# Performance work log

Hardware: AMD Instinct MI355X
Metric: run time of the kernel (lower is better)

## Reference

```python
import jax, jax.numpy as jnp
from jax import lax
import numpy as np

V, B, E, H, T = 32000, 32, 64, 256, 128
START = 0


def setup_inputs() -> dict:
    key = jax.random.key(0)
    ks = jax.random.split(key, 17)
    s = 0.1  # keep logits in a sane range
    inp = {
        "input_x": jax.random.randint(ks[0], (B, T), 0, V, dtype=jnp.int32),
        "emb": jax.random.normal(ks[1], (V, E), jnp.float32) * s,
        "Wi": jax.random.normal(ks[2], (E, H), jnp.float32) * s,
        "Ui": jax.random.normal(ks[3], (H, H), jnp.float32) * s,
        "bi": jax.random.normal(ks[4], (H,), jnp.float32) * s,
        "Wf": jax.random.normal(ks[5], (E, H), jnp.float32) * s,
        "Uf": jax.random.normal(ks[6], (H, H), jnp.float32) * s,
        "bf": jax.random.normal(ks[7], (H,), jnp.float32) * s,
        "Wog": jax.random.normal(ks[8], (E, H), jnp.float32) * s,
        "Uog": jax.random.normal(ks[9], (H, H), jnp.float32) * s,
        "bog": jax.random.normal(ks[10], (H,), jnp.float32) * s,
        "Wc": jax.random.normal(ks[11], (E, H), jnp.float32) * s,
        "Uc": jax.random.normal(ks[12], (H, H), jnp.float32) * s,
        "bc": jax.random.normal(ks[13], (H,), jnp.float32) * s,
        "Wo": jax.random.normal(ks[14], (H, V), jnp.float32) * s,
        "bo": jax.random.normal(ks[15], (V,), jnp.float32) * s,
        "start_token": START,
    }
    return inp


def reference(input_x, emb, Wi, Ui, bi, Wf, Uf, bf, Wog, Uog, bog,
              Wc, Uc, bc, Wo, bo, start_token):
    b, t = input_x.shape
    h_dim = Ui.shape[0]
    # teacher-forcing inputs: [start_emb, emb(x_0..x_{T-2})], time-major [T,B,E]
    x0 = emb[jnp.full((b,), start_token, dtype=jnp.int32)]  # [B,E]
    emb_x = jnp.transpose(emb[input_x], (1, 0, 2))          # [T,B,E]
    xs = jnp.concatenate([x0[None], emb_x[:-1]], axis=0)    # [T,B,E]

    def step(carry, x):
        h, c = carry
        i = jax.nn.sigmoid(x @ Wi + h @ Ui + bi)
        f = jax.nn.sigmoid(x @ Wf + h @ Uf + bf)
        o = jax.nn.sigmoid(x @ Wog + h @ Uog + bog)
        c_bar = jnp.tanh(x @ Wc + h @ Uc + bc)
        c = f * c + i * c_bar
        h = o * jnp.tanh(c)
        logits = h @ Wo + bo                                # [B,V]
        return (h, c), jax.nn.log_softmax(logits, axis=-1)

    h0 = jnp.zeros((b, h_dim), jnp.float32)
    _, logp = lax.scan(step, (h0, h0), xs)                  # [T,B,V]
    logp = jnp.transpose(logp, (1, 0, 2))                   # [B,T,V]
    # -sum over all tokens of log p(target); equals one_hot * log(softmax) sum
    tgt_logp = jnp.take_along_axis(logp, input_x[..., None].astype(jnp.int32), axis=-1)[..., 0]
    return -jnp.sum(tgt_logp)
```

## Files before the change

kernel.cpp:

```cpp
#include <hip/hip_runtime.h>
#include <hip/hip_bf16.h>
#include <math.h>

#define V 32000
#define B 32
#define E 64
#define H 256
#define T 128
#define NROW (B*T)
#define NC 128
#define NVB (V/NC)

typedef __attribute__((ext_vector_type(8))) short bf16x8;
typedef __attribute__((ext_vector_type(4))) float f32x4;
typedef __attribute__((ext_vector_type(8))) unsigned short u16x8;

#define OFF_XS   0
#define OFF_XW   (OFF_XS + NROW*E)
#define OFF_HB   (OFF_XW + NROW*4*H)
#define OFF_PS   (OFF_HB + NROW*H/2)
#define OFF_TL   (OFF_PS + NVB*NROW)
#define OFF_U8   (OFF_TL + NROW)
#define OFF_SC   (OFF_U8 + H*H)
#define OFF_TGT  (OFF_SC + 16)

static __device__ __forceinline__ unsigned short f2bf(float f) {
    union { float f; unsigned int u; } x; x.f = f;
    unsigned int r = x.u + 0x7fffu + ((x.u >> 16) & 1u);
    return (unsigned short)(r >> 16);
}
static __device__ __forceinline__ float bf2f(unsigned short u) {
    union { unsigned int u; float f; } x; x.u = ((unsigned int)u) << 16; return x.f;
}
static __device__ __forceinline__ float sigmoidf_(float x) { return 1.f / (1.f + __expf(-x)); }
static __device__ __forceinline__ float tanhf_(float x)    { return 2.f / (1.f + __expf(-2.f * x)) - 1.f; }

#if defined(__has_builtin)
#if __has_builtin(__builtin_amdgcn_sdot4)
#define HAVE_SDOT4 1
#endif
#endif
static __device__ __forceinline__ int dot4i8(unsigned int a, unsigned int b, int c) {
#ifdef HAVE_SDOT4
    return __builtin_amdgcn_sdot4((int)a, (int)b, c, false);
#else
    c += (int)(char)(a)       * (int)(char)(b);
    c += (int)(char)(a >> 8)  * (int)(char)(b >> 8);
    c += (int)(char)(a >> 16) * (int)(char)(b >> 16);
    c += (int)(char)(a >> 24) * (int)(char)(b >> 24);
    return c;
#endif
}

__global__ void lstm_embed(const int* __restrict__ x, const float* __restrict__ emb,
                           const int* __restrict__ start, float* __restrict__ xs,
                           float* __restrict__ out, int* __restrict__ tgtrow) {
    int idx = blockIdx.x * 256 + threadIdx.x;
    if (idx == 0) out[0] = 0.f;
    if (idx < NROW) tgtrow[idx] = x[(idx & 31) * T + (idx >> 5)];
    if (idx >= T * B * E) return;
    int t   = idx / (B * E);
    int rem = idx - t * (B * E);
    int b   = rem >> 6;
    int e   = rem & 63;
    int tok = (t == 0) ? start[0] : x[b * T + (t - 1)];
    xs[idx] = emb[tok * E + e];
}

__global__ __launch_bounds__(256) void lstm_xw(
        const float* __restrict__ xs, unsigned short* __restrict__ xwq,
        const float* __restrict__ Wi, const float* __restrict__ Wf,
        const float* __restrict__ Wog, const float* __restrict__ Wc,
        const float* __restrict__ bi, const float* __restrict__ bf,
        const float* __restrict__ bog, const float* __restrict__ bc) {
    __shared__ float xsl[32][65];
    const int t = blockIdx.x, tid = threadIdx.x;
    for (int i = tid; i < 32 * 64; i += 256) {
        int b = i >> 6, e = i & 63;
        xsl[b][e] = xs[(size_t)(t * 32 + b) * 64 + e];
    }
    __syncthreads();
    const int b = tid & 31, jg = tid >> 5;
    for (int jj = 0; jj < 32; ++jj) {
        const int j = jg * 32 + jj;
        float a0 = bi[j], a1 = bf[j], a2 = bog[j], a3 = bc[j];
        #pragma unroll 8
        for (int e = 0; e < E; ++e) {
            float xe = xsl[b][e];
            a0 += xe * Wi [e * H + j];
            a1 += xe * Wf [e * H + j];
            a2 += xe * Wog[e * H + j];
            a3 += xe * Wc [e * H + j];
        }
        ushort4 v;
        v.x = f2bf(a0); v.y = f2bf(a1); v.z = f2bf(a2); v.w = f2bf(a3);
        *(ushort4*)(xwq + ((size_t)(t * 32 + b) * 256 + j) * 4) = v;
    }
}

__global__ __launch_bounds__(256) void lstm_umax(
        const float* __restrict__ Ui, const float* __restrict__ Uf,
        const float* __restrict__ Uog, const float* __restrict__ Uc,
        float* __restrict__ sc) {
    const int g = blockIdx.x;
    const float* U = (g == 0) ? Ui : (g == 1) ? Uf : (g == 2) ? Uog : Uc;
    float m = 0.f;
    for (int i = threadIdx.x; i < H * H; i += 256) m = fmaxf(m, fabsf(U[i]));
    __shared__ float red[256];
    red[threadIdx.x] = m;
    __syncthreads();
    for (int off = 128; off > 0; off >>= 1) {
        if (threadIdx.x < off) red[threadIdx.x] = fmaxf(red[threadIdx.x], red[threadIdx.x + off]);
        __syncthreads();
    }
    if (threadIdx.x == 0) sc[g] = fmaxf(red[0], 1e-20f);
}

__global__ __launch_bounds__(256) void lstm_uq8(
        const float* __restrict__ Ui, const float* __restrict__ Uf,
        const float* __restrict__ Uog, const float* __restrict__ Uc,
        const float* __restrict__ sc, unsigned int* __restrict__ UQ8) {
    const int idx = blockIdx.x * 256 + threadIdx.x;
    const int k4 = idx >> 8, j = idx & 255;
    float inv[4] = { 127.f / sc[0], 127.f / sc[1], 127.f / sc[2], 127.f / sc[3] };
    const float* Ug[4] = { Ui, Uf, Uog, Uc };
    uint4 out;
    unsigned int* op = (unsigned int*)&out;
    #pragma unroll
    for (int g = 0; g < 4; ++g) {
        unsigned int w = 0;
        #pragma unroll
        for (int kk = 0; kk < 4; ++kk) {
            float v = Ug[g][(size_t)(k4 * 4 + kk) * H + j];
            int q = __float2int_rn(v * inv[g]);
            q = q > 127 ? 127 : (q < -127 ? -127 : q);
            w |= ((unsigned int)(q & 255)) << (kk * 8);
        }
        op[g] = w;
    }
    *(uint4*)(UQ8 + (size_t)idx * 4) = out;
}

__global__ __launch_bounds__(1024) void lstm_recur_i8(
        const unsigned short* __restrict__ xwq, const uint4* __restrict__ UQ8,
        const float* __restrict__ sc, unsigned short* __restrict__ hb) {
    __shared__ unsigned int hq8[2][64];
    __shared__ int4 red[4][256];
    const int b = blockIdx.x, tid = threadIdx.x;
    const int j = tid & 255, q = tid >> 8;
    const float f0 = sc[0] * (1.f / 16129.f), f1 = sc[1] * (1.f / 16129.f);
    const float f2 = sc[2] * (1.f / 16129.f), f3 = sc[3] * (1.f / 16129.f);
    float c_ = 0.f;

    for (int t = 0; t < T; ++t) {
        if (t > 0) {
            const uint4* up = UQ8 + (size_t)(q * 16) * 256 + j;
            const unsigned int* hrow = hq8[t & 1] + q * 16;
            int a0 = 0, a1 = 0, a2 = 0, a3 = 0;
            #pragma unroll
            for (int m = 0; m < 16; ++m) {
                uint4 u = up[(size_t)m * 256];
                unsigned int hv = hrow[m];
                a0 = dot4i8(u.x, hv, a0);
                a1 = dot4i8(u.y, hv, a1);
                a2 = dot4i8(u.z, hv, a2);
                a3 = dot4i8(u.w, hv, a3);
            }
            red[q][j] = make_int4(a0, a1, a2, a3);
        }
        __syncthreads();
        if (tid < 256) {
            ushort4 xw = *(const ushort4*)(xwq + ((size_t)(t * 32 + b) * 256 + j) * 4);
            float pi = bf2f(xw.x), pf = bf2f(xw.y), po = bf2f(xw.z), pc = bf2f(xw.w);
            if (t > 0) {
                int4 r0 = red[0][j], r1 = red[1][j], r2 = red[2][j], r3 = red[3][j];
                pi += (float)(r0.x + r1.x + r2.x + r3.x) * f0;
                pf += (float)(r0.y + r1.y + r2.y + r3.y) * f1;
                po += (float)(r0.z + r1.z + r2.z + r3.z) * f2;
                pc += (float)(r0.w + r1.w + r2.w + r3.w) * f3;
            }
            c_ = sigmoidf_(pf) * c_ + sigmoidf_(pi) * tanhf_(pc);
            float h = sigmoidf_(po) * tanhf_(c_);
            hb[(size_t)(t * B + b) * H + j] = f2bf(h);
            ((char*)hq8[(t + 1) & 1])[j] = (char)__float2int_rn(h * 127.f);
        }
        __syncthreads();
    }
}

__global__ __launch_bounds__(256) void lstm_wot(const float* __restrict__ Wo,
                                                unsigned short* __restrict__ WoT) {
    __shared__ unsigned short tle[64][65];
    const int n0 = blockIdx.x * 64, k0 = blockIdx.y * 64;
    const int tid = threadIdx.x;
    for (int i = tid; i < 64 * 64; i += 256) {
        int kk = i >> 6, nn = i & 63;
        tle[kk][nn] = f2bf(Wo[(size_t)(k0 + kk) * V + n0 + nn]);
    }
    __syncthreads();
    for (int c = tid; c < 512; c += 256) {
        int nn = c >> 3, kc = c & 7;
        u16x8 v;
        #pragma unroll
        for (int e = 0; e < 8; ++e) v[e] = tle[kc * 8 + e][nn];
        *(u16x8*)(WoT + (size_t)(n0 + nn) * H + k0 + kc * 8) = v;
    }
}

__global__ __launch_bounds__(512, 2) void lstm_logits_mfma(
        const unsigned short* __restrict__ hb, const unsigned short* __restrict__ WoT,
        const float* __restrict__ bo, const int* __restrict__ tgtrow,
        float* __restrict__ ps, float* __restrict__ tl) {
    __shared__ char a_s[65536];
    __shared__ char b_s[65536];
    __shared__ float s_red[4][128];
    __shared__ int   tgt_l[128];
    const int tid = threadIdx.x, lane = tid & 63, wid = tid >> 6;
    const int wr = wid >> 2, wc = wid & 3;
    const int lr = lane & 15, lg = lane >> 4;
    const int swz = lr & 7;
    const int vb = blockIdx.x * NC;

    {
        const uint4* srcB = (const uint4*)(WoT + (size_t)vb * H);
        for (int c = tid; c < 4096; c += 512) {
            int row = c >> 5, c16 = c & 31;
            *(uint4*)(b_s + row * 512 + ((c16 ^ (row & 7)) << 4)) = srcB[c];
        }
    }
    __syncthreads();
    bf16x8 Bf[2][8];
    {
        const char* bBase = b_s + (wc * 32 + lr) * 512;
        #pragma unroll
        for (int nf = 0; nf < 2; ++nf)
            #pragma unroll
            for (int ks = 0; ks < 8; ++ks)
                Bf[nf][ks] = *(const bf16x8*)(bBase + nf * 16 * 512 + (((ks * 4 + lg) ^ swz) << 4));
    }
    float bocol[2] = { bo[vb + wc * 32 + lr], bo[vb + wc * 32 + 16 + lr] };

    for (int rb = 0; rb < NROW / 128; ++rb) {
        {
            const uint4* srcA = (const uint4*)(hb + (size_t)rb * 128 * H);
            for (int c = tid; c < 4096; c += 512) {
                int row = c >> 5, c16 = c & 31;
                *(uint4*)(a_s + row * 512 + ((c16 ^ (row & 7)) << 4)) = srcA[c];
            }
            if (tid < 128) tgt_l[tid] = tgtrow[rb * 128 + tid];
        }
        __syncthreads();

        f32x4 acc[4][2] = {};
        const char* aBase = a_s + (wr * 64 + lr) * 512;
        #pragma unroll
        for (int ks = 0; ks < 8; ++ks) {
            bf16x8 a[4];
            #pragma unroll
            for (int mf = 0; mf < 4; ++mf)
                a[mf] = *(const bf16x8*)(aBase + mf * 16 * 512 + (((ks * 4 + lg) ^ swz) << 4));
            #pragma unroll
            for (int mf = 0; mf < 4; ++mf)
                #pragma unroll
                for (int nf = 0; nf < 2; ++nf)
                    acc[mf][nf] = __builtin_amdgcn_mfma_f32_16x16x32_bf16(a[mf], Bf[nf][ks], acc[mf][nf], 0, 0, 0);
        }

        const int col0 = vb + wc * 32 + lr, col1 = col0 + 16;
        #pragma unroll
        for (int mf = 0; mf < 4; ++mf)
            #pragma unroll
            for (int r = 0; r < 4; ++r) {
                const int row_l = wr * 64 + mf * 16 + lg * 4 + r;
                float v0 = acc[mf][0][r] + bocol[0];
                float v1 = acc[mf][1][r] + bocol[1];
                const int tg = tgt_l[row_l];
                if (tg == col0) tl[rb * 128 + row_l] = v0;
                if (tg == col1) tl[rb * 128 + row_l] = v1;
                float e = __expf(v0) + __expf(v1);
                e += __shfl_xor(e, 1); e += __shfl_xor(e, 2);
                e += __shfl_xor(e, 4); e += __shfl_xor(e, 8);
                if (lr == 0) s_red[wc][row_l] = e;
            }
        __syncthreads();
        if (tid < 128)
            ps[(size_t)blockIdx.x * NROW + rb * 128 + tid] =
                s_red[0][tid] + s_red[1][tid] + s_red[2][tid] + s_red[3][tid];
        __syncthreads();
    }
}

__global__ __launch_bounds__(256) void lstm_lse(
        const float* __restrict__ ps, const float* __restrict__ tl,
        float* __restrict__ out) {
    const int row = blockIdx.x * 256 + threadIdx.x;
    float s = 0.f;
    for (int c = 0; c < NVB; ++c) s += ps[(size_t)c * NROW + row];
    float nll = logf(s) - tl[row];
    __shared__ float red[256];
    red[threadIdx.x] = nll;
    __syncthreads();
    for (int off = 128; off > 0; off >>= 1) {
        if (threadIdx.x < off) red[threadIdx.x] += red[threadIdx.x + off];
        __syncthreads();
    }
    if (threadIdx.x == 0) atomicAdd(out, red[0]);
}

extern "C" void kernel_launch(void* const* d_in, const int* in_sizes, int n_in,
                              void* d_out, int out_size, void* d_ws, size_t ws_size,
                              hipStream_t stream) {
    const int*   x     = (const int*)d_in[0];
    const float* emb   = (const float*)d_in[1];
    const float* Wi    = (const float*)d_in[2];
    const float* Ui    = (const float*)d_in[3];
    const float* bi    = (const float*)d_in[4];
    const float* Wf    = (const float*)d_in[5];
    const float* Uf    = (const float*)d_in[6];
    const float* bf    = (const float*)d_in[7];
    const float* Wog   = (const float*)d_in[8];
    const float* Uog   = (const float*)d_in[9];
    const float* bog   = (const float*)d_in[10];
    const float* Wc    = (const float*)d_in[11];
    const float* Uc    = (const float*)d_in[12];
    const float* bc    = (const float*)d_in[13];
    const float* Wo    = (const float*)d_in[14];
    const float* bo    = (const float*)d_in[15];
    const int*   start = (const int*)d_in[16];
    float* ws  = (float*)d_ws;
    float* out = (float*)d_out;

    float*          xs   = ws + OFF_XS;
    unsigned short* xwq  = (unsigned short*)(ws + OFF_XW);
    unsigned short* WoT  = (unsigned short*)(ws + OFF_XW);
    unsigned short* hbf  = (unsigned short*)(ws + OFF_HB);
    float*          psB  = ws + OFF_PS;
    float*          tlB  = ws + OFF_TL;
    unsigned int*   UQ8  = (unsigned int*)(ws + OFF_U8);
    float*          scB  = ws + OFF_SC;
    int*            tgtr = (int*)(ws + OFF_TGT);

    lstm_embed <<<(T * B * E + 255) / 256, 256, 0, stream>>>(x, emb, start, xs, out, tgtr);
    lstm_xw    <<<T, 256, 0, stream>>>(xs, xwq, Wi, Wf, Wog, Wc, bi, bf, bog, bc);
    lstm_umax  <<<4, 256, 0, stream>>>(Ui, Uf, Uog, Uc, scB);
    lstm_uq8   <<<(H / 4) * H / 256, 256, 0, stream>>>(Ui, Uf, Uog, Uc, scB, UQ8);
    lstm_recur_i8<<<B, 1024, 0, stream>>>(xwq, (const uint4*)UQ8, scB, hbf);
    lstm_wot   <<<dim3(V / 64, H / 64), 256, 0, stream>>>(Wo, WoT);
    lstm_logits_mfma<<<NVB, 512, 0, stream>>>(hbf, WoT, bo, tgtr, psB, tlB);
    lstm_lse   <<<NROW / 256, 256, 0, stream>>>(psB, tlB, out);
}
```

Before: 506.5 us.

## Double-buffer hidden-state tiles in the logits GEMM using direct global-to-LDS loads

The logits MFMA kernel now runs 1024 threads (16 waves, 32 rows each) instead of 512. It double-buffers the 128-row hidden-state A tile across two 64KB LDS buffers, reusing the buffer that first held the Wo^T tile, so loading the next row block overlaps with the MFMAs on the current one. Tiles are staged with global_load_lds when that builtin exists, and the XOR swizzle moves to the global address side. Target ids are now read straight from global memory rather than from an LDS copy. The costs are higher register pressure per wave and a reliance on barriers to wait for the asynchronous LDS loads.

```diff
diff --git a/kernel.cpp b/kernel.cpp
--- a/kernel.cpp
+++ b/kernel.cpp
@@ -38,6 +38,9 @@
 #if defined(__has_builtin)
 #if __has_builtin(__builtin_amdgcn_sdot4)
 #define HAVE_SDOT4 1
+#endif
+#if __has_builtin(__builtin_amdgcn_global_load_lds)
+#define HAVE_GLL 1
 #endif
 #endif
 static __device__ __forceinline__ int dot4i8(unsigned int a, unsigned int b, int c) {
@@ -49,6 +52,16 @@
     c += (int)(char)(a >> 16) * (int)(char)(b >> 16);
     c += (int)(char)(a >> 24) * (int)(char)(b >> 24);
     return c;
+#endif
+}
+static __device__ __forceinline__ void stage16(const char* g, char* l, int lane) {
+#ifdef HAVE_GLL
+    __builtin_amdgcn_global_load_lds(
+        (const __attribute__((address_space(1))) void*)g,
+        (__attribute__((address_space(3))) void*)l, 16, 0, 0);
+    (void)lane;
+#else
+    *(uint4*)(l + lane * 16) = *(const uint4*)g;
 #endif
 }
 
@@ -207,31 +220,33 @@
     }
 }
 
-__global__ __launch_bounds__(512, 2) void lstm_logits_mfma(
+__global__ __launch_bounds__(1024, 4) void lstm_logits_mfma(
         const unsigned short* __restrict__ hb, const unsigned short* __restrict__ WoT,
         const float* __restrict__ bo, const int* __restrict__ tgtrow,
         float* __restrict__ ps, float* __restrict__ tl) {
-    __shared__ char a_s[65536];
-    __shared__ char b_s[65536];
-    __shared__ float s_red[4][128];
-    __shared__ int   tgt_l[128];
+    __shared__ char ab0[65536];
+    __shared__ char ab1[65536];
+    __shared__ float s_red[4][132];
     const int tid = threadIdx.x, lane = tid & 63, wid = tid >> 6;
     const int wr = wid >> 2, wc = wid & 3;
     const int lr = lane & 15, lg = lane >> 4;
     const int swz = lr & 7;
     const int vb = blockIdx.x * NC;
 
-    {
-        const uint4* srcB = (const uint4*)(WoT + (size_t)vb * H);
-        for (int c = tid; c < 4096; c += 512) {
-            int row = c >> 5, c16 = c & 31;
-            *(uint4*)(b_s + row * 512 + ((c16 ^ (row & 7)) << 4)) = srcB[c];
-        }
-    }
+    #define STAGE_TILE(dst_, srcbase_) { _Pragma("unroll") \
+        for (int i_ = 0; i_ < 4; ++i_) { \
+            int chunk_ = (wid * 4 + i_) * 64 + lane; \
+            int row_ = chunk_ >> 5, c16_ = chunk_ & 31; \
+            int srcc_ = c16_ ^ (row_ & 7); \
+            stage16((const char*)(srcbase_) + row_ * 512 + srcc_ * 16, \
+                    (dst_) + (wid * 4 + i_) * 1024, lane); \
+        } }
+
+    STAGE_TILE(ab0, (const char*)(WoT + (size_t)vb * H));
     __syncthreads();
     bf16x8 Bf[2][8];
     {
-        const char* bBase = b_s + (wc * 32 + lr) * 512;
+        const char* bBase = ab0 + (wc * 32 + lr) * 512;
         #pragma unroll
         for (int nf = 0; nf < 2; ++nf)
             #pragma unroll
@@ -239,42 +254,37 @@
                 Bf[nf][ks] = *(const bf16x8*)(bBase + nf * 16 * 512 + (((ks * 4 + lg) ^ swz) << 4));
     }
     float bocol[2] = { bo[vb + wc * 32 + lr], bo[vb + wc * 32 + 16 + lr] };
+    STAGE_TILE(ab1, (const char*)hb);
+    __syncthreads();
 
     for (int rb = 0; rb < NROW / 128; ++rb) {
-        {
-            const uint4* srcA = (const uint4*)(hb + (size_t)rb * 128 * H);
-            for (int c = tid; c < 4096; c += 512) {
-                int row = c >> 5, c16 = c & 31;
-                *(uint4*)(a_s + row * 512 + ((c16 ^ (row & 7)) << 4)) = srcA[c];
-            }
-            if (tid < 128) tgt_l[tid] = tgtrow[rb * 128 + tid];
-        }
-        __syncthreads();
-
-        f32x4 acc[4][2] = {};
-        const char* aBase = a_s + (wr * 64 + lr) * 512;
+        char* curb = (rb & 1) ? ab0 : ab1;
+        char* nxtb = (rb & 1) ? ab1 : ab0;
+        if (rb + 1 < NROW / 128)
+            STAGE_TILE(nxtb, (const char*)(hb + (size_t)(rb + 1) * 128 * H));
+
+        f32x4 acc[2][2] = {};
+        const char* aBase = curb + (wr * 32 + lr) * 512;
         #pragma unroll
         for (int ks = 0; ks < 8; ++ks) {
-            bf16x8 a[4];
-            #pragma unroll
-            for (int mf = 0; mf < 4; ++mf)
-                a[mf] = *(const bf16x8*)(aBase + mf * 16 * 512 + (((ks * 4 + lg) ^ swz) << 4));
-            #pragma unroll
-            for (int mf = 0; mf < 4; ++mf)
-                #pragma unroll
-                for (int nf = 0; nf < 2; ++nf)
-                    acc[mf][nf] = __builtin_amdgcn_mfma_f32_16x16x32_bf16(a[mf], Bf[nf][ks], acc[mf][nf], 0, 0, 0);
+            const int co = ((ks * 4 + lg) ^ swz) << 4;
+            bf16x8 a0 = *(const bf16x8*)(aBase + co);
+            bf16x8 a1 = *(const bf16x8*)(aBase + 16 * 512 + co);
+            acc[0][0] = __builtin_amdgcn_mfma_f32_16x16x32_bf16(a0, Bf[0][ks], acc[0][0], 0, 0, 0);
+            acc[0][1] = __builtin_amdgcn_mfma_f32_16x16x32_bf16(a0, Bf[1][ks], acc[0][1], 0, 0, 0);
+            acc[1][0] = __builtin_amdgcn_mfma_f32_16x16x32_bf16(a1, Bf[0][ks], acc[1][0], 0, 0, 0);
+            acc[1][1] = __builtin_amdgcn_mfma_f32_16x16x32_bf16(a1, Bf[1][ks], acc[1][1], 0, 0, 0);
         }
 
         const int col0 = vb + wc * 32 + lr, col1 = col0 + 16;
         #pragma unroll
-        for (int mf = 0; mf < 4; ++mf)
+        for (int mf = 0; mf < 2; ++mf)
             #pragma unroll
             for (int r = 0; r < 4; ++r) {
-                const int row_l = wr * 64 + mf * 16 + lg * 4 + r;
+                const int row_l = wr * 32 + mf * 16 + lg * 4 + r;
                 float v0 = acc[mf][0][r] + bocol[0];
                 float v1 = acc[mf][1][r] + bocol[1];
-                const int tg = tgt_l[row_l];
+                const int tg = tgtrow[rb * 128 + row_l];
                 if (tg == col0) tl[rb * 128 + row_l] = v0;
                 if (tg == col1) tl[rb * 128 + row_l] = v1;
                 float e = __expf(v0) + __expf(v1);
@@ -288,6 +298,7 @@
                 s_red[0][tid] + s_red[1][tid] + s_red[2][tid] + s_red[3][tid];
         __syncthreads();
     }
+    #undef STAGE_TILE
 }
 
 __global__ __launch_bounds__(256) void lstm_lse(
@@ -346,6 +357,6 @@
     lstm_uq8   <<<(H / 4) * H / 256, 256, 0, stream>>>(Ui, Uf, Uog, Uc, scB, UQ8);
     lstm_recur_i8<<<B, 1024, 0, stream>>>(xwq, (const uint4*)UQ8, scB, hbf);
     lstm_wot   <<<dim3(V / 64, H / 64), 256, 0, stream>>>(Wo, WoT);
-    lstm_logits_mfma<<<NVB, 512, 0, stream>>>(hbf, WoT, bo, tgtr, psB, tlB);
+    lstm_logits_mfma<<<NVB, 1024, 0, stream>>>(hbf, WoT, bo, tgtr, psB, tlB);
     lstm_lse   <<<NROW / 256, 256, 0, stream>>>(psB, tlB, out);
 }
```

New measurement: 438.4 us. 13.4% less time.
